# Optimization experiments

Hardware: AMD Instinct MI355X
Metric: run time of the kernel (lower is better)

## Reference

```python
import jax, jax.numpy as jnp
import numpy as np

N, E, F, H = 50000, 800000, 128, 128
HEADS, HOUT, NUM_GRAPHS, NUM_CLASSES, L = 4, 32, 50, 2, 3
BN_EPS = 1e-5


def setup_inputs() -> dict:
    key = jax.random.key(0)
    it = iter(jax.random.split(key, 64))
    def nrm(shape, scale=0.1):
        return scale * jax.random.normal(next(it), shape, jnp.float32)
    npg = N // NUM_GRAPHS  # nodes per graph = 1000
    # edges constrained to stay within a single graph
    src = jax.random.randint(next(it), (E,), 0, npg, jnp.int32)
    dst = jax.random.randint(next(it), (E,), 0, npg, jnp.int32)
    goff = jax.random.randint(next(it), (E,), 0, NUM_GRAPHS, jnp.int32) * npg
    return dict(
        x=jax.random.normal(next(it), (N, F), jnp.float32),
        edge_index=jnp.stack([src + goff, dst + goff]),
        batch=jnp.arange(N, dtype=jnp.int32) // npg,
        W_gcn=nrm((F, H)), b_gcn=nrm((H,)),
        gin_W1=nrm((F, H)), gin_b1=nrm((H,)), gin_W2=nrm((H, H)), gin_b2=nrm((H,)),
        W_gat=nrm((F, HEADS * HOUT)), b_gat=nrm((HEADS * HOUT,)),
        a_src=nrm((HEADS, HOUT)), a_dst=nrm((HEADS, HOUT)),
        gat_proj_W=nrm((HEADS * HOUT, H)), gat_proj_b=nrm((H,)),
        gate_W1=nrm((3 * H, H)), gate_b1=nrm((H,)), gate_W2=nrm((H, 3)), gate_b2=nrm((3,)),
        bn0_g=jnp.ones((H,), jnp.float32) + nrm((H,)), bn0_b=nrm((H,)),
        conv_rel_W=nrm((L, H, H)), conv_rel_b=nrm((L, H)), conv_root_W=nrm((L, H, H)),
        bn_g=jnp.ones((L, H), jnp.float32) + nrm((L, H)), bn_b=nrm((L, H)),
        jump_W=nrm((L * H, H)), jump_b=nrm((H,)),
        att_W1=nrm((H, H)), att_b1=nrm((H,)), att_W2=nrm((H, 1)), att_b2=nrm((1,)),
        comb_W=nrm((4 * H, H)), comb_b=nrm((H,)),
        cls_W1=nrm((H, H // 2)), cls_b1=nrm((H // 2,)),
        cls_W2=nrm((H // 2, NUM_CLASSES)), cls_b2=nrm((NUM_CLASSES,)),
    )


def _forward(x, edge_index, batch, W_gcn, b_gcn, gin_W1, gin_b1, gin_W2, gin_b2,
             W_gat, b_gat, a_src, a_dst, gat_proj_W, gat_proj_b,
             gate_W1, gate_b1, gate_W2, gate_b2, bn0_g, bn0_b,
             conv_rel_W, conv_rel_b, conv_root_W, bn_g, bn_b, jump_W, jump_b,
             att_W1, att_b1, att_W2, att_b2, comb_W, comb_b,
             cls_W1, cls_b1, cls_W2, cls_b2):
    relu = jax.nn.relu
    seg_sum, seg_max = jax.ops.segment_sum, jax.ops.segment_max
    n = x.shape[0]
    src, dst = edge_index[0], edge_index[1]
    loop = jnp.arange(n, dtype=src.dtype)
    src_sl = jnp.concatenate([src, loop])  # self-loops (GCN/GAT add them)
    dst_sl = jnp.concatenate([dst, loop])

    def bn(h, g, b):  # eval-mode BatchNorm1d, running mean=0, var=1
        return h * (g / jnp.sqrt(1.0 + BN_EPS)) + b

    # --- GCN stem: sym-normalized A+I ---
    deg = seg_sum(jnp.ones_like(dst_sl, jnp.float32), dst_sl, num_segments=n)
    dinv = jax.lax.rsqrt(deg)  # deg >= 1 thanks to self-loops
    norm = dinv[src_sl] * dinv[dst_sl]
    h = x @ W_gcn
    x_gcn = relu(seg_sum(h[src_sl] * norm[:, None], dst_sl, num_segments=n) + b_gcn)

    # --- GIN stem: MLP((1+0)*x + sum_j x_j), no self-loops ---
    aggr = seg_sum(x[src], dst, num_segments=n)
    x_gin = relu(relu((x + aggr) @ gin_W1 + gin_b1) @ gin_W2 + gin_b2)

    # --- GAT stem: per-edge attention, segment softmax over dst ---
    xp = (x @ W_gat).reshape(n, HEADS, HOUT)
    al_s = (xp * a_src).sum(-1)  # [n, heads]
    al_d = (xp * a_dst).sum(-1)
    e = jax.nn.leaky_relu(al_s[src_sl] + al_d[dst_sl], 0.2)  # [E+n, heads]
    m = seg_max(e, dst_sl, num_segments=n)
    ex = jnp.exp(e - m[dst_sl])
    alpha = ex / seg_sum(ex, dst_sl, num_segments=n)[dst_sl]
    x_gat = seg_sum(xp[src_sl] * alpha[:, :, None], dst_sl, num_segments=n)
    x_gat = x_gat.reshape(n, HEADS * HOUT) + b_gat
    x_gat = relu(x_gat) @ gat_proj_W + gat_proj_b

    # --- gated fusion ---
    x_cat = jnp.concatenate([x_gcn, x_gin, x_gat], axis=-1)
    gates = jax.nn.softmax(relu(x_cat @ gate_W1 + gate_b1) @ gate_W2 + gate_b2, axis=-1)
    xx = gates[:, 0:1] * x_gcn + gates[:, 1:2] * x_gin + gates[:, 2:3] * x_gat
    xx = relu(bn(xx, bn0_g, bn0_b))  # dropout = no-op in eval

    # --- GraphConv stack with residuals (IdentityPooling since use_sag=False) ---
    reps = []
    for i in range(L):
        x_in = xx
        a = seg_sum(xx[src], dst, num_segments=n)  # aggr='add'
        h = a @ conv_rel_W[i] + conv_rel_b[i] + xx @ conv_root_W[i]
        xx = relu(bn(h, bn_g[i], bn_b[i])) + x_in
        reps.append(xx)

    xx = jnp.concatenate(reps, axis=-1) @ jump_W + jump_b  # JK cat

    # --- combo global pooling: mean / max / add / att ---
    cnt = seg_sum(jnp.ones((n,), jnp.float32), batch, num_segments=NUM_GRAPHS)
    x_add = seg_sum(xx, batch, num_segments=NUM_GRAPHS)
    x_mean = x_add / cnt[:, None]
    x_max = seg_max(xx, batch, num_segments=NUM_GRAPHS)
    a_log = (relu(xx @ att_W1 + att_b1) @ att_W2 + att_b2)[:, 0]  # [n]
    mg = seg_max(a_log, batch, num_segments=NUM_GRAPHS)
    exg = jnp.exp(a_log - mg[batch])
    att = exg / seg_sum(exg, batch, num_segments=NUM_GRAPHS)[batch]
    x_att = seg_sum(xx * att[:, None], batch, num_segments=NUM_GRAPHS)
    hg = jnp.concatenate([x_mean, x_max, x_add, x_att], axis=-1) @ comb_W + comb_b

    return relu(hg @ cls_W1 + cls_b1) @ cls_W2 + cls_b2  # [NUM_GRAPHS, NUM_CLASSES]


def reference(x, edge_index, batch, W_gcn, b_gcn, gin_W1, gin_b1, gin_W2, gin_b2,
              W_gat, b_gat, a_src, a_dst, gat_proj_W, gat_proj_b,
              gate_W1, gate_b1, gate_W2, gate_b2, bn0_g, bn0_b,
              conv_rel_W, conv_rel_b, conv_root_W, bn_g, bn_b, jump_W, jump_b,
              att_W1, att_b1, att_W2, att_b2, comb_W, comb_b,
              cls_W1, cls_b1, cls_W2, cls_b2):
    return _forward(x, edge_index, batch, W_gcn, b_gcn, gin_W1, gin_b1, gin_W2, gin_b2,
                    W_gat, b_gat, a_src, a_dst, gat_proj_W, gat_proj_b,
                    gate_W1, gate_b1, gate_W2, gate_b2, bn0_g, bn0_b,
                    conv_rel_W, conv_rel_b, conv_root_W, bn_g, bn_b, jump_W, jump_b,
                    att_W1, att_b1, att_W2, att_b2, comb_W, comb_b,
                    cls_W1, cls_b1, cls_W2, cls_b2)
```

## Files before the change

kernel.cpp:

```cpp
#include <hip/hip_runtime.h>

typedef float f32x4 __attribute__((ext_vector_type(4)));
typedef short s16x8 __attribute__((ext_vector_type(8)));

#define LDA 136

static __device__ __forceinline__ unsigned short f2bf(float f){
  union { float f; unsigned int u; } v; v.f = f;
  unsigned int u = v.u;
  return (unsigned short)((u + 0x7fffu + ((u >> 16) & 1u)) >> 16);
}
static __device__ __forceinline__ float2 bfp2f(unsigned int p){
  union { unsigned int u; float f; } a, b;
  a.u = (p & 0xffffu) << 16; b.u = p & 0xffff0000u;
  return make_float2(a.f, b.f);
}
static __device__ __forceinline__ unsigned int f2bfp(float x, float y){
  return (unsigned int)f2bf(x) | ((unsigned int)f2bf(y) << 16);
}
static __device__ __forceinline__ float bf2f(unsigned short h){
  union { unsigned int u; float f; } v; v.u = (unsigned int)h << 16; return v.f;
}

static __device__ __forceinline__ float lrelu02(float x){ return x > 0.f ? x : 0.2f * x; }

static __device__ __forceinline__ int xcd_swz(int bid, int nwg){
  int q = nwg >> 3, r = nwg & 7, x = bid & 7, i = bid >> 3;
  return (x < r ? x * (q + 1) : r * (q + 1) + (x - r) * q) + i;
}


__global__ void zero_u32(unsigned int* p, int n){
  int i = blockIdx.x * 256 + threadIdx.x;
  if (i < n) p[i] = 0u;
}

__global__ void hist_kernel(const int* __restrict__ dst, unsigned int* __restrict__ cnt, int E){
  int i = blockIdx.x * 256 + threadIdx.x;
  if (i < E) atomicAdd(&cnt[dst[i]], 1u);
}

__global__ void scan1_kernel(const unsigned int* __restrict__ cnt, unsigned int* __restrict__ rp,
                             unsigned int* __restrict__ bsum, int n){
  __shared__ unsigned int s[1024];
  int b = blockIdx.x, tid = threadIdx.x, i = b * 1024 + tid;
  unsigned int v = (i < n) ? cnt[i] : 0u;
  s[tid] = v; __syncthreads();
  for (int off = 1; off < 1024; off <<= 1){
    unsigned int t = (tid >= off) ? s[tid - off] : 0u;
    __syncthreads();
    s[tid] += t;
    __syncthreads();
  }
  if (i < n) rp[i] = s[tid] - v;
  if (tid == 1023) bsum[b] = s[1023];
}

__global__ void scan2_kernel(unsigned int* __restrict__ bsum, int nb){
  __shared__ unsigned int s[256];
  int tid = threadIdx.x;
  unsigned int v = (tid < nb) ? bsum[tid] : 0u;
  s[tid] = v; __syncthreads();
  for (int off = 1; off < 256; off <<= 1){
    unsigned int t = (tid >= off) ? s[tid - off] : 0u;
    __syncthreads();
    s[tid] += t;
    __syncthreads();
  }
  if (tid < nb) bsum[tid] = s[tid] - v;
}

__global__ void scan3_kernel(unsigned int* __restrict__ rp, const unsigned int* __restrict__ bsum,
                             int n, unsigned int Etot){
  int i = blockIdx.x * 256 + threadIdx.x;
  if (i < n) rp[i] += bsum[i >> 10];
  if (i == 0) rp[n] = Etot;
}

__global__ void scatter_kernel(const int* __restrict__ src, const int* __restrict__ dst,
                               const unsigned int* __restrict__ rp, unsigned int* __restrict__ fill,
                               int* __restrict__ colA, int* __restrict__ cpos, int E){
  int i = blockIdx.x * 256 + threadIdx.x;
  if (i < E){
    int d = dst[i];
    unsigned int pos = rp[d] + atomicAdd(&fill[d], 1u);
    colA[pos] = src[i];
    cpos[i] = (int)pos;
  }
}

__global__ void dinv_kernel(const unsigned int* __restrict__ cnt, float* __restrict__ dinv, int n){
  int i = blockIdx.x * 256 + threadIdx.x;
  if (i < n) dinv[i] = rsqrtf((float)cnt[i] + 1.0f);
}

__global__ void xcast_kernel(const float* __restrict__ x, unsigned short* __restrict__ xb, int n2){
  int i = blockIdx.x * 256 + threadIdx.x;
  if (i < n2){
    float2 v = ((const float2*)x)[i];
    ((unsigned int*)xb)[i] = f2bfp(v.x, v.y);
  }
}

__global__ void ew_kernel(const int* __restrict__ src, const int* __restrict__ dst,
                          const int* __restrict__ cpos, const float* __restrict__ als,
                          const float* __restrict__ ald, float* __restrict__ wCSR, int E){
  int i = blockIdx.x * 256 + threadIdx.x;
  if (i >= E) return;
  int s = src[i], d = dst[i];
  float4 as = ((const float4*)als)[s];
  float4 ad = ((const float4*)ald)[d];
  float4 w;
  w.x = __expf(fminf(lrelu02(as.x + ad.x), 30.f));
  w.y = __expf(fminf(lrelu02(as.y + ad.y), 30.f));
  w.z = __expf(fminf(lrelu02(as.z + ad.z), 30.f));
  w.w = __expf(fminf(lrelu02(as.w + ad.w), 30.f));
  ((float4*)wCSR)[cpos[i]] = w;
}


struct WSrc { const float* p[18]; };

__global__ void wtrans_kernel(WSrc s, unsigned short* __restrict__ dstAll){
  const float* src = s.p[blockIdx.x];
  unsigned short* dst = dstAll + (size_t)blockIdx.x * 16384;
  __shared__ float st[64][129];
  int tid = threadIdx.x;
  int kb = blockIdx.y * 64;
#pragma unroll
  for (int j = 0; j < 8; ++j){
    int e = tid + 256 * j;
    int r = e >> 5, c4 = (e & 31) * 4;
    float4 v = *(const float4*)(src + (size_t)(kb + r) * 128 + c4);
    st[r][c4] = v.x; st[r][c4+1] = v.y; st[r][c4+2] = v.z; st[r][c4+3] = v.w;
  }
  __syncthreads();
#pragma unroll
  for (int j = 0; j < 8; ++j){
    int e = tid + 256 * j;
    int c = e >> 4, k4 = (e & 15) * 4;
    ushort4 o;
    o.x = f2bf(st[k4+0][c]); o.y = f2bf(st[k4+1][c]);
    o.z = f2bf(st[k4+2][c]); o.w = f2bf(st[k4+3][c]);
    *(ushort4*)(dst + (size_t)c * 128 + kb + k4) = o;
  }
}


template<int EPI>
__launch_bounds__(256, 2)
__global__ void gemm_kernel(const unsigned short* __restrict__ A0, const unsigned short* __restrict__ A1,
                            const unsigned short* __restrict__ A2,
                            const unsigned short* __restrict__ W0, const unsigned short* __restrict__ W1,
                            const unsigned short* __restrict__ W2,
                            const float* __restrict__ bias, const float* __restrict__ bng, const float* __restrict__ bnb,
                            const unsigned short* __restrict__ resid, unsigned short* __restrict__ C, int nrows)
{
  __shared__ unsigned short As[64 * LDA];
  __shared__ unsigned short Wt[128 * LDA];
  const int tid = threadIdx.x;
  const int wave = tid >> 6, lane = tid & 63;
  const int row0 = blockIdx.x * 64;
  const unsigned short* Aps[3] = {A0, A1, A2};
  const unsigned short* Wps[3] = {W0, W1, W2};
  f32x4 acc[8];
#pragma unroll
  for (int i = 0; i < 8; ++i) acc[i] = (f32x4){0.f, 0.f, 0.f, 0.f};

  for (int p = 0; p < 3; ++p){
    const unsigned short* Ap = Aps[p];
    if (Ap == nullptr) break;
    const unsigned short* Wp = Wps[p];
    if (p) __syncthreads();
#pragma unroll
    for (int j = 0; j < 4; ++j){
      int e = tid + 256 * j;
      int r = e >> 4, k8 = (e & 15) * 8;
      int gr = row0 + r;
      s16x8 v = {0,0,0,0,0,0,0,0};
      if (gr < nrows) v = *(const s16x8*)(Ap + (size_t)gr * 128 + k8);
      *(s16x8*)(As + r * LDA + k8) = v;
    }
#pragma unroll
    for (int j = 0; j < 8; ++j){
      int e = tid + 256 * j;
      int colw = e >> 4, k8 = (e & 15) * 8;
      *(s16x8*)(Wt + colw * LDA + k8) = *(const s16x8*)(Wp + (size_t)colw * 128 + k8);
    }
    __syncthreads();
#pragma unroll
    for (int kc = 0; kc < 4; ++kc){
      int ko = kc * 32 + (lane >> 4) * 8;
      s16x8 av = *(const s16x8*)(As + (wave * 16 + (lane & 15)) * LDA + ko);
#pragma unroll
      for (int ct = 0; ct < 8; ++ct){
        s16x8 bv = *(const s16x8*)(Wt + (ct * 16 + (lane & 15)) * LDA + ko);
        acc[ct] = __builtin_amdgcn_mfma_f32_16x16x32_bf16(av, bv, acc[ct], 0, 0, 0);
      }
    }
  }
  const float RSQ = 0.99999500003749969f;
#pragma unroll
  for (int ct = 0; ct < 8; ++ct){
    int colg = ct * 16 + (lane & 15);
    float bv_ = (EPI >= 1) ? bias[colg] : 0.f;
    float sg = (EPI == 3) ? bng[colg] * RSQ : 0.f;
    float sb = (EPI == 3) ? bnb[colg] : 0.f;
#pragma unroll
    for (int r = 0; r < 4; ++r){
      int rowg = row0 + wave * 16 + (lane >> 4) * 4 + r;
      if (rowg < nrows){
        float v = acc[ct][r];
        if (EPI == 1) v += bv_;
        else if (EPI == 2) v = fmaxf(v + bv_, 0.f);
        else if (EPI == 3){
          v = (v + bv_) * sg + sb;
          v = fmaxf(v, 0.f) + bf2f(resid[(size_t)rowg * 128 + colg]);
        }
        C[(size_t)rowg * 128 + colg] = f2bf(v);
      }
    }
  }
}

__launch_bounds__(256, 2)
__global__ void gemm_dual_kernel(const unsigned short* __restrict__ A,
                                 const unsigned short* __restrict__ W0, const unsigned short* __restrict__ W1,
                                 const float* __restrict__ dscale,
                                 unsigned short* __restrict__ C0, unsigned short* __restrict__ C1, int nrows)
{
  __shared__ unsigned short As[64 * LDA];
  __shared__ unsigned short Wt[128 * LDA];
  const int tid = threadIdx.x;
  const int wave = tid >> 6, lane = tid & 63;
  const int row0 = blockIdx.x * 64;
  f32x4 acc0[8], acc1[8];
#pragma unroll
  for (int i = 0; i < 8; ++i){ acc0[i] = (f32x4){0.f,0.f,0.f,0.f}; acc1[i] = (f32x4){0.f,0.f,0.f,0.f}; }

#pragma unroll
  for (int j = 0; j < 4; ++j){
    int e = tid + 256 * j;
    int r = e >> 4, k8 = (e & 15) * 8;
    int gr = row0 + r;
    s16x8 v = {0,0,0,0,0,0,0,0};
    if (gr < nrows) v = *(const s16x8*)(A + (size_t)gr * 128 + k8);
    *(s16x8*)(As + r * LDA + k8) = v;
  }
#pragma unroll
  for (int j = 0; j < 8; ++j){
    int e = tid + 256 * j;
    int colw = e >> 4, k8 = (e & 15) * 8;
    *(s16x8*)(Wt + colw * LDA + k8) = *(const s16x8*)(W0 + (size_t)colw * 128 + k8);
  }
  __syncthreads();
  s16x8 av[4];
#pragma unroll
  for (int kc = 0; kc < 4; ++kc)
    av[kc] = *(const s16x8*)(As + (wave * 16 + (lane & 15)) * LDA + kc * 32 + (lane >> 4) * 8);
#pragma unroll
  for (int kc = 0; kc < 4; ++kc){
    int ko = kc * 32 + (lane >> 4) * 8;
#pragma unroll
    for (int ct = 0; ct < 8; ++ct){
      s16x8 bv = *(const s16x8*)(Wt + (ct * 16 + (lane & 15)) * LDA + ko);
      acc0[ct] = __builtin_amdgcn_mfma_f32_16x16x32_bf16(av[kc], bv, acc0[ct], 0, 0, 0);
    }
  }
  __syncthreads();
#pragma unroll
  for (int j = 0; j < 8; ++j){
    int e = tid + 256 * j;
    int colw = e >> 4, k8 = (e & 15) * 8;
    *(s16x8*)(Wt + colw * LDA + k8) = *(const s16x8*)(W1 + (size_t)colw * 128 + k8);
  }
  __syncthreads();
#pragma unroll
  for (int kc = 0; kc < 4; ++kc){
    int ko = kc * 32 + (lane >> 4) * 8;
#pragma unroll
    for (int ct = 0; ct < 8; ++ct){
      s16x8 bv = *(const s16x8*)(Wt + (ct * 16 + (lane & 15)) * LDA + ko);
      acc1[ct] = __builtin_amdgcn_mfma_f32_16x16x32_bf16(av[kc], bv, acc1[ct], 0, 0, 0);
    }
  }
#pragma unroll
  for (int ct = 0; ct < 8; ++ct){
    int colg = ct * 16 + (lane & 15);
#pragma unroll
    for (int r = 0; r < 4; ++r){
      int rowg = row0 + wave * 16 + (lane >> 4) * 4 + r;
      if (rowg < nrows){
        C0[(size_t)rowg * 128 + colg] = f2bf(acc0[ct][r] * dscale[rowg]);
        C1[(size_t)rowg * 128 + colg] = f2bf(acc1[ct][r]);
      }
    }
  }
}


__global__ void gin_agg_kernel(const unsigned short* __restrict__ x, const unsigned int* __restrict__ rp,
                               const int* __restrict__ col, unsigned short* __restrict__ xs, int n){
  int bid = xcd_swz(blockIdx.x, gridDim.x);
  int node = bid * 4 + (int)(threadIdx.x >> 6);
  if (node >= n) return;
  int lane = threadIdx.x & 63;
  const unsigned int* xin = (const unsigned int*)x;
  float2 acc = bfp2f(xin[(size_t)node * 64 + lane]);
  unsigned int rs = rp[node], re = rp[node + 1], e = rs;
  for (; e + 4 <= re; e += 4){
    int s0 = col[e], s1 = col[e+1], s2 = col[e+2], s3 = col[e+3];
    float2 v0 = bfp2f(xin[(size_t)s0 * 64 + lane]);
    float2 v1 = bfp2f(xin[(size_t)s1 * 64 + lane]);
    float2 v2 = bfp2f(xin[(size_t)s2 * 64 + lane]);
    float2 v3 = bfp2f(xin[(size_t)s3 * 64 + lane]);
    acc.x += v0.x + v1.x + v2.x + v3.x;
    acc.y += v0.y + v1.y + v2.y + v3.y;
  }
  for (; e < re; ++e){
    float2 v = bfp2f(xin[(size_t)col[e] * 64 + lane]);
    acc.x += v.x; acc.y += v.y;
  }
  ((unsigned int*)xs)[(size_t)node * 64 + lane] = f2bfp(acc.x, acc.y);
}

__global__ void gcn_agg_kernel(const unsigned short* __restrict__ hd, const float* __restrict__ dinv,
                               const unsigned int* __restrict__ rp, const int* __restrict__ col,
                               const float* __restrict__ b, unsigned short* __restrict__ out, int n){
  int bid = xcd_swz(blockIdx.x, gridDim.x);
  int node = bid * 4 + (int)(threadIdx.x >> 6);
  if (node >= n) return;
  int lane = threadIdx.x & 63;
  const unsigned int* hv = (const unsigned int*)hd;
  float di = dinv[node];
  float2 acc = bfp2f(hv[(size_t)node * 64 + lane]);
  unsigned int rs = rp[node], re = rp[node + 1], e = rs;
  for (; e + 4 <= re; e += 4){
    int s0 = col[e], s1 = col[e+1], s2 = col[e+2], s3 = col[e+3];
    float2 v0 = bfp2f(hv[(size_t)s0 * 64 + lane]);
    float2 v1 = bfp2f(hv[(size_t)s1 * 64 + lane]);
    float2 v2 = bfp2f(hv[(size_t)s2 * 64 + lane]);
    float2 v3 = bfp2f(hv[(size_t)s3 * 64 + lane]);
    acc.x += v0.x + v1.x + v2.x + v3.x;
    acc.y += v0.y + v1.y + v2.y + v3.y;
  }
  for (; e < re; ++e){
    float2 v = bfp2f(hv[(size_t)col[e] * 64 + lane]);
    acc.x += v.x; acc.y += v.y;
  }
  int f = lane * 2;
  float o0 = fmaxf(acc.x * di + b[f], 0.f);
  float o1 = fmaxf(acc.y * di + b[f + 1], 0.f);
  ((unsigned int*)out)[(size_t)node * 64 + lane] = f2bfp(o0, o1);
}

__global__ void sum_agg_kernel(const unsigned short* __restrict__ x, const unsigned int* __restrict__ rp,
                               const int* __restrict__ col, unsigned short* __restrict__ out, int n){
  int bid = xcd_swz(blockIdx.x, gridDim.x);
  int node = bid * 4 + (int)(threadIdx.x >> 6);
  if (node >= n) return;
  int lane = threadIdx.x & 63;
  const unsigned int* xin = (const unsigned int*)x;
  float2 acc = make_float2(0.f, 0.f);
  unsigned int rs = rp[node], re = rp[node + 1], e = rs;
  for (; e + 4 <= re; e += 4){
    int s0 = col[e], s1 = col[e+1], s2 = col[e+2], s3 = col[e+3];
    float2 v0 = bfp2f(xin[(size_t)s0 * 64 + lane]);
    float2 v1 = bfp2f(xin[(size_t)s1 * 64 + lane]);
    float2 v2 = bfp2f(xin[(size_t)s2 * 64 + lane]);
    float2 v3 = bfp2f(xin[(size_t)s3 * 64 + lane]);
    acc.x += v0.x + v1.x + v2.x + v3.x;
    acc.y += v0.y + v1.y + v2.y + v3.y;
  }
  for (; e < re; ++e){
    float2 v = bfp2f(xin[(size_t)col[e] * 64 + lane]);
    acc.x += v.x; acc.y += v.y;
  }
  ((unsigned int*)out)[(size_t)node * 64 + lane] = f2bfp(acc.x, acc.y);
}

__global__ void gat_agg_kernel(const unsigned short* __restrict__ xp, const float* __restrict__ als,
                               const float* __restrict__ ald, const float* __restrict__ wCSR,
                               const unsigned int* __restrict__ rp, const int* __restrict__ col,
                               const float* __restrict__ bgat, unsigned short* __restrict__ out, int n){
  int bid = xcd_swz(blockIdx.x, gridDim.x);
  int node = bid * 4 + (int)(threadIdx.x >> 6);
  if (node >= n) return;
  int lane = threadIdx.x & 63;
  int h = lane >> 4;
  const unsigned int* xv = (const unsigned int*)xp;
  float w = __expf(fminf(lrelu02(als[(size_t)node * 4 + h] + ald[(size_t)node * 4 + h]), 30.f));
  float2 sv = bfp2f(xv[(size_t)node * 64 + lane]);
  float2 acc = make_float2(sv.x * w, sv.y * w);
  float denom = w;
  unsigned int rs = rp[node], re = rp[node + 1], e = rs;
  for (; e + 4 <= re; e += 4){
    int s0 = col[e], s1 = col[e+1], s2 = col[e+2], s3 = col[e+3];
    float w0 = wCSR[(size_t)(e+0) * 4 + h];
    float w1 = wCSR[(size_t)(e+1) * 4 + h];
    float w2 = wCSR[(size_t)(e+2) * 4 + h];
    float w3 = wCSR[(size_t)(e+3) * 4 + h];
    float2 v0 = bfp2f(xv[(size_t)s0 * 64 + lane]);
    float2 v1 = bfp2f(xv[(size_t)s1 * 64 + lane]);
    float2 v2 = bfp2f(xv[(size_t)s2 * 64 + lane]);
    float2 v3 = bfp2f(xv[(size_t)s3 * 64 + lane]);
    acc.x += v0.x * w0 + v1.x * w1 + v2.x * w2 + v3.x * w3;
    acc.y += v0.y * w0 + v1.y * w1 + v2.y * w2 + v3.y * w3;
    denom += w0 + w1 + w2 + w3;
  }
  for (; e < re; ++e){
    float we = wCSR[(size_t)e * 4 + h];
    float2 v = bfp2f(xv[(size_t)col[e] * 64 + lane]);
    acc.x += v.x * we; acc.y += v.y * we;
    denom += we;
  }
  float inv = 1.0f / denom;
  int f = lane * 2;
  float o0 = fmaxf(acc.x * inv + bgat[f], 0.f);
  float o1 = fmaxf(acc.y * inv + bgat[f + 1], 0.f);
  ((unsigned int*)out)[(size_t)node * 64 + lane] = f2bfp(o0, o1);
}


__global__ void alpair_kernel(const unsigned short* __restrict__ xp, const float* __restrict__ a_src,
                              const float* __restrict__ a_dst, float* __restrict__ als,
                              float* __restrict__ ald, int n){
  int node = blockIdx.x * 4 + (int)(threadIdx.x >> 6);
  if (node >= n) return;
  int lane = threadIdx.x & 63;
  int f = lane * 2;
  float2 v = bfp2f(((const unsigned int*)xp)[(size_t)node * 64 + lane]);
  float ps = v.x * a_src[f] + v.y * a_src[f + 1];
  float pd = v.x * a_dst[f] + v.y * a_dst[f + 1];
#pragma unroll
  for (int off = 1; off < 16; off <<= 1){
    ps += __shfl_xor(ps, off, 64);
    pd += __shfl_xor(pd, off, 64);
  }
  if ((lane & 15) == 0){
    int hh = lane >> 4;
    als[(size_t)node * 4 + hh] = ps;
    ald[(size_t)node * 4 + hh] = pd;
  }
}

__global__ void combine_kernel(const unsigned short* __restrict__ t, const float* __restrict__ W2,
                               const float* __restrict__ b2, const unsigned short* __restrict__ xg,
                               const unsigned short* __restrict__ xi, const unsigned short* __restrict__ xa,
                               const float* __restrict__ bn0g, const float* __restrict__ bn0b,
                               unsigned short* __restrict__ xx, int n){
  int node = blockIdx.x * 4 + (int)(threadIdx.x >> 6);
  if (node >= n) return;
  int lane = threadIdx.x & 63;
  int f = lane * 2;
  float2 tv = bfp2f(((const unsigned int*)t)[(size_t)node * 64 + lane]);
  float p0 = tv.x * W2[f * 3 + 0] + tv.y * W2[(f + 1) * 3 + 0];
  float p1 = tv.x * W2[f * 3 + 1] + tv.y * W2[(f + 1) * 3 + 1];
  float p2 = tv.x * W2[f * 3 + 2] + tv.y * W2[(f + 1) * 3 + 2];
#pragma unroll
  for (int off = 1; off < 64; off <<= 1){
    p0 += __shfl_xor(p0, off, 64);
    p1 += __shfl_xor(p1, off, 64);
    p2 += __shfl_xor(p2, off, 64);
  }
  p0 += b2[0]; p1 += b2[1]; p2 += b2[2];
  float mm = fmaxf(p0, fmaxf(p1, p2));
  float e0 = __expf(p0 - mm), e1 = __expf(p1 - mm), e2 = __expf(p2 - mm);
  float inv = 1.0f / (e0 + e1 + e2);
  e0 *= inv; e1 *= inv; e2 *= inv;
  float2 a = bfp2f(((const unsigned int*)xg)[(size_t)node * 64 + lane]);
  float2 b = bfp2f(((const unsigned int*)xi)[(size_t)node * 64 + lane]);
  float2 c = bfp2f(((const unsigned int*)xa)[(size_t)node * 64 + lane]);
  const float RSQ = 0.99999500003749969f;
  float o0 = fmaxf((e0 * a.x + e1 * b.x + e2 * c.x) * (bn0g[f] * RSQ) + bn0b[f], 0.f);
  float o1 = fmaxf((e0 * a.y + e1 * b.y + e2 * c.y) * (bn0g[f + 1] * RSQ) + bn0b[f + 1], 0.f);
  ((unsigned int*)xx)[(size_t)node * 64 + lane] = f2bfp(o0, o1);
}

__global__ void alog_kernel(const unsigned short* __restrict__ t, const float* __restrict__ w,
                            const float* __restrict__ b, float* __restrict__ alog, int n){
  int node = blockIdx.x * 4 + (int)(threadIdx.x >> 6);
  if (node >= n) return;
  int lane = threadIdx.x & 63;
  int f = lane * 2;
  float2 tv = bfp2f(((const unsigned int*)t)[(size_t)node * 64 + lane]);
  float p = tv.x * w[f] + tv.y * w[f + 1];
#pragma unroll
  for (int off = 1; off < 64; off <<= 1) p += __shfl_xor(p, off, 64);
  if (lane == 0) alog[node] = p + b[0];
}


__global__ void att_stats_kernel(const float* __restrict__ alog, float* __restrict__ gm,
                                 float* __restrict__ gz, int npg){
  __shared__ float red[256];
  int g = blockIdx.x, tid = threadIdx.x;
  size_t base = (size_t)g * npg;
  float m = -1e30f;
  for (int i = tid; i < npg; i += 256) m = fmaxf(m, alog[base + i]);
  red[tid] = m; __syncthreads();
  for (int off = 128; off > 0; off >>= 1){ if (tid < off) red[tid] = fmaxf(red[tid], red[tid + off]); __syncthreads(); }
  float gmax = red[0]; __syncthreads();
  float z = 0.f;
  for (int i = tid; i < npg; i += 256) z += __expf(alog[base + i] - gmax);
  red[tid] = z; __syncthreads();
  for (int off = 128; off > 0; off >>= 1){ if (tid < off) red[tid] += red[tid + off]; __syncthreads(); }
  if (tid == 0){ gm[g] = gmax; gz[g] = red[0]; }
}

__global__ void pool_partial_kernel(const unsigned short* __restrict__ xx, const float* __restrict__ alog,
                                    const float* __restrict__ gm, const float* __restrict__ gz,
                                    float* __restrict__ part, int npg, int nparts){
  __shared__ float wts[128];
  __shared__ float red[256];
  int g = blockIdx.x / nparts, p = blockIdx.x % nparts;
  int chunk = (npg + nparts - 1) / nparts;
  int n0 = p * chunk, n1 = min(npg, n0 + chunk);
  int tid = threadIdx.x;
  float gmax = gm[g], ginv = 1.0f / gz[g];
  size_t base = (size_t)g * npg;
  for (int i = n0 + tid; i < n1; i += 256) wts[i - n0] = __expf(alog[base + i] - gmax) * ginv;
  __syncthreads();
  int f = tid & 127, half = tid >> 7;
  float add = 0.f, mx = -1e30f, att = 0.f;
  for (int n2 = n0 + half; n2 < n1; n2 += 2){
    float v = bf2f(xx[(base + n2) * 128 + f]);
    add += v; mx = fmaxf(mx, v); att += v * wts[n2 - n0];
  }
  red[tid] = add; __syncthreads();
  float addf = add + ((half == 0) ? red[tid + 128] : 0.f);
  __syncthreads(); red[tid] = mx; __syncthreads();
  float mxf = (half == 0) ? fmaxf(mx, red[tid + 128]) : 0.f;
  __syncthreads(); red[tid] = att; __syncthreads();
  float attf = att + ((half == 0) ? red[tid + 128] : 0.f);
  if (half == 0){
    float* o = part + (size_t)(g * nparts + p) * 384;
    o[f] = addf; o[128 + f] = mxf; o[256 + f] = attf;
  }
}

__global__ void pool_final_kernel(const float* __restrict__ part, float* __restrict__ hg,
                                  int npg, int nparts){
  int g = blockIdx.x, f = threadIdx.x;
  float add = 0.f, mx = -1e30f, att = 0.f;
  for (int p = 0; p < nparts; ++p){
    const float* o = part + (size_t)(g * nparts + p) * 384;
    add += o[f]; mx = fmaxf(mx, o[128 + f]); att += o[256 + f];
  }
  float* o = hg + (size_t)g * 512;
  o[f] = add / (float)npg;
  o[128 + f] = mx;
  o[256 + f] = add;
  o[384 + f] = att;
}

__global__ void head_kernel(const float* __restrict__ hg, const float* __restrict__ combW,
                            const float* __restrict__ combB, const float* __restrict__ c1W,
                            const float* __restrict__ c1B, const float* __restrict__ c2W,
                            const float* __restrict__ c2B, float* __restrict__ out){
  __shared__ float cat[512];
  __shared__ float h1[128];
  __shared__ float h2[64];
  int g = blockIdx.x, tid = threadIdx.x;
#pragma unroll
  for (int j = 0; j < 4; ++j) cat[tid + 128 * j] = hg[(size_t)g * 512 + tid + 128 * j];
  __syncthreads();
  float a = combB[tid];
  for (int k = 0; k < 512; ++k) a += cat[k] * combW[(size_t)k * 128 + tid];
  h1[tid] = a; __syncthreads();
  if (tid < 64){
    float b = c1B[tid];
    for (int k = 0; k < 128; ++k) b += h1[k] * c1W[(size_t)k * 64 + tid];
    h2[tid] = fmaxf(b, 0.f);
  }
  __syncthreads();
  if (tid < 2){
    float o = c2B[tid];
    for (int k = 0; k < 64; ++k) o += h2[k] * c2W[(size_t)k * 2 + tid];
    out[(size_t)g * 2 + tid] = o;
  }
}


static void launch_gemm(int epi, dim3 grid, hipStream_t st,
                        const unsigned short* A0, const unsigned short* A1, const unsigned short* A2,
                        const unsigned short* W0, const unsigned short* W1, const unsigned short* W2,
                        const float* bias, const float* bng, const float* bnb,
                        const unsigned short* resid, unsigned short* C, int nrows){
  switch (epi){
    case 0: gemm_kernel<0><<<grid, 256, 0, st>>>(A0, A1, A2, W0, W1, W2, bias, bng, bnb, resid, C, nrows); break;
    case 1: gemm_kernel<1><<<grid, 256, 0, st>>>(A0, A1, A2, W0, W1, W2, bias, bng, bnb, resid, C, nrows); break;
    case 2: gemm_kernel<2><<<grid, 256, 0, st>>>(A0, A1, A2, W0, W1, W2, bias, bng, bnb, resid, C, nrows); break;
    default: gemm_kernel<3><<<grid, 256, 0, st>>>(A0, A1, A2, W0, W1, W2, bias, bng, bnb, resid, C, nrows); break;
  }
}

extern "C" void kernel_launch(void* const* d_in, const int* in_sizes, int n_in,
                              void* d_out, int out_size, void* d_ws, size_t ws_size,
                              hipStream_t stream){
  (void)n_in; (void)out_size; (void)ws_size;
  const int N = in_sizes[0] / 128;
  const int E = in_sizes[1] / 2;
  const int NG = 50;
  const int npg = N / NG;

  const float* x       = (const float*)d_in[0];
  const int*   ei      = (const int*)d_in[1];
  const int*   srcI    = ei;
  const int*   dstI    = ei + E;
  const float* W_gcn   = (const float*)d_in[3];
  const float* b_gcn   = (const float*)d_in[4];
  const float* gin_W1  = (const float*)d_in[5];
  const float* gin_b1  = (const float*)d_in[6];
  const float* gin_W2  = (const float*)d_in[7];
  const float* gin_b2  = (const float*)d_in[8];
  const float* W_gat   = (const float*)d_in[9];
  const float* b_gat   = (const float*)d_in[10];
  const float* a_src   = (const float*)d_in[11];
  const float* a_dst   = (const float*)d_in[12];
  const float* gproj_W = (const float*)d_in[13];
  const float* gproj_b = (const float*)d_in[14];
  const float* gate_W1 = (const float*)d_in[15];
  const float* gate_b1 = (const float*)d_in[16];
  const float* gate_W2 = (const float*)d_in[17];
  const float* gate_b2 = (const float*)d_in[18];
  const float* bn0_g   = (const float*)d_in[19];
  const float* bn0_b   = (const float*)d_in[20];
  const float* rel_W   = (const float*)d_in[21];
  const float* rel_b   = (const float*)d_in[22];
  const float* root_W  = (const float*)d_in[23];
  const float* bn_g    = (const float*)d_in[24];
  const float* bn_b    = (const float*)d_in[25];
  const float* jump_W  = (const float*)d_in[26];
  const float* jump_b  = (const float*)d_in[27];
  const float* att_W1  = (const float*)d_in[28];
  const float* att_b1  = (const float*)d_in[29];
  const float* att_W2  = (const float*)d_in[30];
  const float* att_b2  = (const float*)d_in[31];
  const float* comb_W  = (const float*)d_in[32];
  const float* comb_b  = (const float*)d_in[33];
  const float* cls_W1  = (const float*)d_in[34];
  const float* cls_b1  = (const float*)d_in[35];
  const float* cls_W2  = (const float*)d_in[36];
  const float* cls_b2  = (const float*)d_in[37];
  float* out = (float*)d_out;

  char* wp = (char*)d_ws;
  auto alloc = [&](size_t b) -> char* {
    char* p = wp; wp += (b + 511) & ~(size_t)511; return p;
  };
  unsigned int* cnt  = (unsigned int*)alloc((size_t)N * 4);
  unsigned int* fill = (unsigned int*)alloc((size_t)N * 4);
  unsigned int* rp   = (unsigned int*)alloc(((size_t)N + 1) * 4);
  int* colA          = (int*)alloc((size_t)E * 4);
  int* cpos          = (int*)alloc((size_t)E * 4);
  float* wCSR        = (float*)alloc((size_t)E * 16);
  unsigned int* bsum = (unsigned int*)alloc(256 * 4);
  float* dinv        = (float*)alloc((size_t)N * 4);
  float* als         = (float*)alloc((size_t)N * 16);
  float* ald         = (float*)alloc((size_t)N * 16);
  float* alogv       = (float*)alloc((size_t)N * 4);
  unsigned short* WtAll = (unsigned short*)alloc((size_t)18 * 16384 * 2);
  float* hg          = (float*)alloc((size_t)NG * 512 * 4);
  float* gmv         = (float*)alloc((size_t)NG * 4);
  float* gzv         = (float*)alloc((size_t)NG * 4);
  int nparts = (npg + 99) / 100;
  float* part        = (float*)alloc((size_t)NG * nparts * 384 * 4);
  unsigned short* xbf = (unsigned short*)alloc((size_t)N * 128 * 2);
  unsigned short* S0 = (unsigned short*)alloc((size_t)N * 128 * 2);
  unsigned short* S1 = (unsigned short*)alloc((size_t)N * 128 * 2);
  unsigned short* S2 = (unsigned short*)alloc((size_t)N * 128 * 2);
  unsigned short* S3 = (unsigned short*)alloc((size_t)N * 128 * 2);
  unsigned short* S4 = (unsigned short*)alloc((size_t)N * 128 * 2);

  int zn = (int)(((char*)rp - (char*)cnt) / 4);
  zero_u32<<<(zn + 255) / 256, 256, 0, stream>>>(cnt, zn);
  hist_kernel<<<(E + 255) / 256, 256, 0, stream>>>(dstI, cnt, E);
  int nbScan = (N + 1023) / 1024;
  scan1_kernel<<<nbScan, 1024, 0, stream>>>(cnt, rp, bsum, N);
  scan2_kernel<<<1, 256, 0, stream>>>(bsum, nbScan);
  scan3_kernel<<<(N + 255) / 256, 256, 0, stream>>>(rp, bsum, N, (unsigned int)E);
  scatter_kernel<<<(E + 255) / 256, 256, 0, stream>>>(srcI, dstI, rp, fill, colA, cpos, E);
  dinv_kernel<<<(N + 255) / 256, 256, 0, stream>>>(cnt, dinv, N);

  WSrc wsrc;
  wsrc.p[0] = W_gcn;  wsrc.p[1] = W_gat;  wsrc.p[2] = gin_W1; wsrc.p[3] = gin_W2;
  wsrc.p[4] = gproj_W;
  wsrc.p[5] = gate_W1;      wsrc.p[6] = gate_W1 + 16384; wsrc.p[7] = gate_W1 + 32768;
  wsrc.p[8] = rel_W;        wsrc.p[9] = rel_W + 16384;   wsrc.p[10] = rel_W + 32768;
  wsrc.p[11] = root_W;      wsrc.p[12] = root_W + 16384; wsrc.p[13] = root_W + 32768;
  wsrc.p[14] = jump_W;      wsrc.p[15] = jump_W + 16384; wsrc.p[16] = jump_W + 32768;
  wsrc.p[17] = att_W1;
  wtrans_kernel<<<dim3(18, 2), 256, 0, stream>>>(wsrc, WtAll);
  xcast_kernel<<<(N * 64 + 255) / 256, 256, 0, stream>>>(x, xbf, N * 64);

  dim3 gg((N + 63) / 64);
  int nb4 = (N + 3) / 4;
  #define WT(i) (WtAll + (size_t)(i) * 16384)
  const unsigned short* Z = nullptr;
  const unsigned short* BZ = nullptr;

  gemm_dual_kernel<<<gg, 256, 0, stream>>>(xbf, WT(0), WT(1), dinv, S0, S1, N);
  alpair_kernel<<<nb4, 256, 0, stream>>>(S1, a_src, a_dst, als, ald, N);
  ew_kernel<<<(E + 255) / 256, 256, 0, stream>>>(srcI, dstI, cpos, als, ald, wCSR, E);
  gin_agg_kernel<<<nb4, 256, 0, stream>>>(xbf, rp, colA, S2, N);
  launch_gemm(2, gg, stream, S2, BZ, BZ, WT(2), Z, Z, gin_b1, nullptr, nullptr, BZ, S3, N);
  launch_gemm(2, gg, stream, S3, BZ, BZ, WT(3), Z, Z, gin_b2, nullptr, nullptr, BZ, S2, N);
  gcn_agg_kernel<<<nb4, 256, 0, stream>>>(S0, dinv, rp, colA, b_gcn, S3, N);
  gat_agg_kernel<<<nb4, 256, 0, stream>>>(S1, als, ald, wCSR, rp, colA, b_gat, S0, N);
  launch_gemm(1, gg, stream, S0, BZ, BZ, WT(4), Z, Z, gproj_b, nullptr, nullptr, BZ, S1, N);

  launch_gemm(2, gg, stream, S3, S2, S1, WT(5), WT(6), WT(7), gate_b1, nullptr, nullptr, BZ, S4, N);
  combine_kernel<<<nb4, 256, 0, stream>>>(S4, gate_W2, gate_b2, S3, S2, S1, bn0_g, bn0_b, S0, N);

  sum_agg_kernel<<<nb4, 256, 0, stream>>>(S0, rp, colA, S1, N);
  launch_gemm(3, gg, stream, S1, S0, BZ, WT(8), WT(11), Z, rel_b, bn_g, bn_b, S0, S2, N);
  sum_agg_kernel<<<nb4, 256, 0, stream>>>(S2, rp, colA, S1, N);
  launch_gemm(3, gg, stream, S1, S2, BZ, WT(9), WT(12), Z, rel_b + 128, bn_g + 128, bn_b + 128, S2, S3, N);
  sum_agg_kernel<<<nb4, 256, 0, stream>>>(S3, rp, colA, S1, N);
  launch_gemm(3, gg, stream, S1, S3, BZ, WT(10), WT(13), Z, rel_b + 256, bn_g + 256, bn_b + 256, S3, S4, N);

  launch_gemm(1, gg, stream, S2, S3, S4, WT(14), WT(15), WT(16), jump_b, nullptr, nullptr, BZ, S0, N);
  launch_gemm(2, gg, stream, S0, BZ, BZ, WT(17), Z, Z, att_b1, nullptr, nullptr, BZ, S1, N);
  alog_kernel<<<nb4, 256, 0, stream>>>(S1, att_W2, att_b2, alogv, N);

  att_stats_kernel<<<NG, 256, 0, stream>>>(alogv, gmv, gzv, npg);
  pool_partial_kernel<<<NG * nparts, 256, 0, stream>>>(S0, alogv, gmv, gzv, part, npg, nparts);
  pool_final_kernel<<<NG, 128, 0, stream>>>(part, hg, npg, nparts);
  head_kernel<<<NG, 128, 0, stream>>>(hg, comb_W, comb_b, cls_W1, cls_b1, cls_W2, cls_b2, out);
}
```

Baseline: 693.1 us.

## Build CSR per graph with two-level bucketing and store GAT edge weights in bf16

Replaces the global histogram, three-pass scan and atomic scatter with per-graph bucketing. Edges are first bucketed by graph, then each graph's CSR is built in one block using shared-memory histograms and a block scan, which also writes dinv and a per-edge destination array. The edge-weight kernel now walks edges in CSR order (no cpos indirection) and stores the four head weights as bf16. This cuts global atomics, kernel launches and edge-weight bandwidth. In exchange it relies on edges never crossing graphs and on npg being at most 1024, and it loses precision in the attention weights.

```diff
diff --git a/kernel.cpp b/kernel.cpp
--- a/kernel.cpp
+++ b/kernel.cpp
@@ -35,63 +35,88 @@
   if (i < n) p[i] = 0u;
 }
 
-__global__ void hist_kernel(const int* __restrict__ dst, unsigned int* __restrict__ cnt, int E){
-  int i = blockIdx.x * 256 + threadIdx.x;
-  if (i < E) atomicAdd(&cnt[dst[i]], 1u);
-}
-
-__global__ void scan1_kernel(const unsigned int* __restrict__ cnt, unsigned int* __restrict__ rp,
-                             unsigned int* __restrict__ bsum, int n){
-  __shared__ unsigned int s[1024];
-  int b = blockIdx.x, tid = threadIdx.x, i = b * 1024 + tid;
-  unsigned int v = (i < n) ? cnt[i] : 0u;
-  s[tid] = v; __syncthreads();
+__global__ void gcount_kernel(const int* __restrict__ dst, unsigned int* __restrict__ gcnt,
+                              int E, int npg, int ng){
+  __shared__ unsigned int h[64];
+  int tid = threadIdx.x;
+  if (tid < 64) h[tid] = 0u;
+  __syncthreads();
+  for (int i = blockIdx.x * 256 + tid; i < E; i += gridDim.x * 256)
+    atomicAdd(&h[dst[i] / npg], 1u);
+  __syncthreads();
+  if (tid < ng) atomicAdd(&gcnt[tid], h[tid]);
+}
+
+__global__ void gscan_kernel(const unsigned int* __restrict__ gcnt, unsigned int* __restrict__ goff, int ng){
+  if (threadIdx.x == 0){
+    unsigned int run = 0;
+    for (int i = 0; i < ng; ++i){ goff[i] = run; run += gcnt[i]; }
+    goff[ng] = run;
+  }
+}
+
+__global__ void gbucket_kernel(const int* __restrict__ src, const int* __restrict__ dst,
+                               const unsigned int* __restrict__ goff, unsigned int* __restrict__ gfill,
+                               int2* __restrict__ ebuf, int E, int npg, int ng){
+  __shared__ unsigned int h[64];
+  __shared__ unsigned int base[64];
+  __shared__ unsigned int fl[64];
+  int tid = threadIdx.x;
+  if (tid < 64){ h[tid] = 0u; fl[tid] = 0u; }
+  __syncthreads();
+  int per = (E + gridDim.x - 1) / gridDim.x;
+  int i0 = blockIdx.x * per, i1 = min(E, i0 + per);
+  for (int i = i0 + tid; i < i1; i += 256)
+    atomicAdd(&h[dst[i] / npg], 1u);
+  __syncthreads();
+  if (tid < ng) base[tid] = goff[tid] + atomicAdd(&gfill[tid], h[tid]);
+  __syncthreads();
+  for (int i = i0 + tid; i < i1; i += 256){
+    int d = dst[i];
+    int g = d / npg;
+    unsigned int p = base[g] + atomicAdd(&fl[g], 1u);
+    ebuf[p] = make_int2(src[i], d);
+  }
+}
+
+__global__ void csr_graph_kernel(const int2* __restrict__ ebuf, const unsigned int* __restrict__ goff,
+                                 unsigned int* __restrict__ rp, int* __restrict__ colA,
+                                 int* __restrict__ dstA, float* __restrict__ dinv,
+                                 int npg, int N, int Etot){
+  __shared__ unsigned int hist[1024];
+  __shared__ unsigned int fill[1024];
+  int g = blockIdx.x, tid = threadIdx.x;
+  unsigned int e0 = goff[g], e1 = goff[g + 1];
+  int nbase = g * npg;
+  hist[tid] = 0u; fill[tid] = 0u;
+  __syncthreads();
+  for (unsigned int e = e0 + tid; e < e1; e += 1024)
+    atomicAdd(&hist[ebuf[e].y - nbase], 1u);
+  __syncthreads();
+  unsigned int cnt = hist[tid];
   for (int off = 1; off < 1024; off <<= 1){
-    unsigned int t = (tid >= off) ? s[tid - off] : 0u;
+    unsigned int t = (tid >= off) ? hist[tid - off] : 0u;
     __syncthreads();
-    s[tid] += t;
+    hist[tid] += t;
     __syncthreads();
   }
-  if (i < n) rp[i] = s[tid] - v;
-  if (tid == 1023) bsum[b] = s[1023];
-}
-
-__global__ void scan2_kernel(unsigned int* __restrict__ bsum, int nb){
-  __shared__ unsigned int s[256];
-  int tid = threadIdx.x;
-  unsigned int v = (tid < nb) ? bsum[tid] : 0u;
-  s[tid] = v; __syncthreads();
-  for (int off = 1; off < 256; off <<= 1){
-    unsigned int t = (tid >= off) ? s[tid - off] : 0u;
-    __syncthreads();
-    s[tid] += t;
-    __syncthreads();
-  }
-  if (tid < nb) bsum[tid] = s[tid] - v;
-}
-
-__global__ void scan3_kernel(unsigned int* __restrict__ rp, const unsigned int* __restrict__ bsum,
-                             int n, unsigned int Etot){
-  int i = blockIdx.x * 256 + threadIdx.x;
-  if (i < n) rp[i] += bsum[i >> 10];
-  if (i == 0) rp[n] = Etot;
-}
-
-__global__ void scatter_kernel(const int* __restrict__ src, const int* __restrict__ dst,
-                               const unsigned int* __restrict__ rp, unsigned int* __restrict__ fill,
-                               int* __restrict__ colA, int* __restrict__ cpos, int E){
-  int i = blockIdx.x * 256 + threadIdx.x;
-  if (i < E){
-    int d = dst[i];
-    unsigned int pos = rp[d] + atomicAdd(&fill[d], 1u);
-    colA[pos] = src[i];
-    cpos[i] = (int)pos;
-  }
-}
-
-__global__ void dinv_kernel(const unsigned int* __restrict__ cnt, float* __restrict__ dinv, int n){
-  int i = blockIdx.x * 256 + threadIdx.x;
-  if (i < n) dinv[i] = rsqrtf((float)cnt[i] + 1.0f);
+  unsigned int basev = e0 + hist[tid] - cnt;
+  __syncthreads();
+  hist[tid] = basev;
+  if (tid < npg){
+    int node = nbase + tid;
+    rp[node] = basev;
+    dinv[node] = rsqrtf((float)cnt + 1.0f);
+  }
+  if (g == 0 && tid == 0) rp[N] = (unsigned int)Etot;
+  __syncthreads();
+  for (unsigned int e = e0 + tid; e < e1; e += 1024){
+    int2 sd = ebuf[e];
+    int ld = sd.y - nbase;
+    unsigned int pos = hist[ld] + atomicAdd(&fill[ld], 1u);
+    colA[pos] = sd.x;
+    dstA[pos] = sd.y;
+  }
 }
 
 __global__ void xcast_kernel(const float* __restrict__ x, unsigned short* __restrict__ xb, int n2){
@@ -102,20 +127,20 @@
   }
 }
 
-__global__ void ew_kernel(const int* __restrict__ src, const int* __restrict__ dst,
-                          const int* __restrict__ cpos, const float* __restrict__ als,
-                          const float* __restrict__ ald, float* __restrict__ wCSR, int E){
+__global__ void ew_kernel(const int* __restrict__ colA, const int* __restrict__ dstA,
+                          const float* __restrict__ als, const float* __restrict__ ald,
+                          unsigned int* __restrict__ wb, int E){
   int i = blockIdx.x * 256 + threadIdx.x;
   if (i >= E) return;
-  int s = src[i], d = dst[i];
+  int s = colA[i], d = dstA[i];
   float4 as = ((const float4*)als)[s];
   float4 ad = ((const float4*)ald)[d];
-  float4 w;
-  w.x = __expf(fminf(lrelu02(as.x + ad.x), 30.f));
-  w.y = __expf(fminf(lrelu02(as.y + ad.y), 30.f));
-  w.z = __expf(fminf(lrelu02(as.z + ad.z), 30.f));
-  w.w = __expf(fminf(lrelu02(as.w + ad.w), 30.f));
-  ((float4*)wCSR)[cpos[i]] = w;
+  float w0 = __expf(fminf(lrelu02(as.x + ad.x), 30.f));
+  float w1 = __expf(fminf(lrelu02(as.y + ad.y), 30.f));
+  float w2 = __expf(fminf(lrelu02(as.z + ad.z), 30.f));
+  float w3 = __expf(fminf(lrelu02(as.w + ad.w), 30.f));
+  wb[(size_t)i * 2 + 0] = f2bfp(w0, w1);
+  wb[(size_t)i * 2 + 1] = f2bfp(w2, w3);
 }
 
 
@@ -380,7 +405,7 @@
 }
 
 __global__ void gat_agg_kernel(const unsigned short* __restrict__ xp, const float* __restrict__ als,
-                               const float* __restrict__ ald, const float* __restrict__ wCSR,
+                               const float* __restrict__ ald, const unsigned int* __restrict__ wb,
                                const unsigned int* __restrict__ rp, const int* __restrict__ col,
                                const float* __restrict__ bgat, unsigned short* __restrict__ out, int n){
   int bid = xcd_swz(blockIdx.x, gridDim.x);
@@ -388,6 +413,7 @@
   if (node >= n) return;
   int lane = threadIdx.x & 63;
   int h = lane >> 4;
+  int wword = h >> 1, wsh = (h & 1) * 16;
   const unsigned int* xv = (const unsigned int*)xp;
   float w = __expf(fminf(lrelu02(als[(size_t)node * 4 + h] + ald[(size_t)node * 4 + h]), 30.f));
   float2 sv = bfp2f(xv[(size_t)node * 64 + lane]);
@@ -396,10 +422,10 @@
   unsigned int rs = rp[node], re = rp[node + 1], e = rs;
   for (; e + 4 <= re; e += 4){
     int s0 = col[e], s1 = col[e+1], s2 = col[e+2], s3 = col[e+3];
-    float w0 = wCSR[(size_t)(e+0) * 4 + h];
-    float w1 = wCSR[(size_t)(e+1) * 4 + h];
-    float w2 = wCSR[(size_t)(e+2) * 4 + h];
-    float w3 = wCSR[(size_t)(e+3) * 4 + h];
+    float w0 = bf2f((unsigned short)(wb[(size_t)(e+0) * 2 + wword] >> wsh));
+    float w1 = bf2f((unsigned short)(wb[(size_t)(e+1) * 2 + wword] >> wsh));
+    float w2 = bf2f((unsigned short)(wb[(size_t)(e+2) * 2 + wword] >> wsh));
+    float w3 = bf2f((unsigned short)(wb[(size_t)(e+3) * 2 + wword] >> wsh));
     float2 v0 = bfp2f(xv[(size_t)s0 * 64 + lane]);
     float2 v1 = bfp2f(xv[(size_t)s1 * 64 + lane]);
     float2 v2 = bfp2f(xv[(size_t)s2 * 64 + lane]);
@@ -409,7 +435,7 @@
     denom += w0 + w1 + w2 + w3;
   }
   for (; e < re; ++e){
-    float we = wCSR[(size_t)e * 4 + h];
+    float we = bf2f((unsigned short)(wb[(size_t)e * 2 + wword] >> wsh));
     float2 v = bfp2f(xv[(size_t)col[e] * 64 + lane]);
     acc.x += v.x * we; acc.y += v.y * we;
     denom += we;
@@ -649,13 +675,14 @@
   auto alloc = [&](size_t b) -> char* {
     char* p = wp; wp += (b + 511) & ~(size_t)511; return p;
   };
-  unsigned int* cnt  = (unsigned int*)alloc((size_t)N * 4);
-  unsigned int* fill = (unsigned int*)alloc((size_t)N * 4);
   unsigned int* rp   = (unsigned int*)alloc(((size_t)N + 1) * 4);
   int* colA          = (int*)alloc((size_t)E * 4);
-  int* cpos          = (int*)alloc((size_t)E * 4);
-  float* wCSR        = (float*)alloc((size_t)E * 16);
-  unsigned int* bsum = (unsigned int*)alloc(256 * 4);
+  int* dstA          = (int*)alloc((size_t)E * 4);
+  int2* ebuf         = (int2*)alloc((size_t)E * 8);
+  unsigned int* wb   = (unsigned int*)alloc((size_t)E * 8);
+  unsigned int* gcnt = (unsigned int*)alloc(192 * 4);
+  unsigned int* gfill= gcnt + 64;
+  unsigned int* goff = gcnt + 128;
   float* dinv        = (float*)alloc((size_t)N * 4);
   float* als         = (float*)alloc((size_t)N * 16);
   float* ald         = (float*)alloc((size_t)N * 16);
@@ -673,15 +700,11 @@
   unsigned short* S3 = (unsigned short*)alloc((size_t)N * 128 * 2);
   unsigned short* S4 = (unsigned short*)alloc((size_t)N * 128 * 2);
 
-  int zn = (int)(((char*)rp - (char*)cnt) / 4);
-  zero_u32<<<(zn + 255) / 256, 256, 0, stream>>>(cnt, zn);
-  hist_kernel<<<(E + 255) / 256, 256, 0, stream>>>(dstI, cnt, E);
-  int nbScan = (N + 1023) / 1024;
-  scan1_kernel<<<nbScan, 1024, 0, stream>>>(cnt, rp, bsum, N);
-  scan2_kernel<<<1, 256, 0, stream>>>(bsum, nbScan);
-  scan3_kernel<<<(N + 255) / 256, 256, 0, stream>>>(rp, bsum, N, (unsigned int)E);
-  scatter_kernel<<<(E + 255) / 256, 256, 0, stream>>>(srcI, dstI, rp, fill, colA, cpos, E);
-  dinv_kernel<<<(N + 255) / 256, 256, 0, stream>>>(cnt, dinv, N);
+  zero_u32<<<1, 256, 0, stream>>>(gcnt, 128);
+  gcount_kernel<<<256, 256, 0, stream>>>(dstI, gcnt, E, npg, NG);
+  gscan_kernel<<<1, 64, 0, stream>>>(gcnt, goff, NG);
+  gbucket_kernel<<<256, 256, 0, stream>>>(srcI, dstI, goff, gfill, ebuf, E, npg, NG);
+  csr_graph_kernel<<<NG, 1024, 0, stream>>>(ebuf, goff, rp, colA, dstA, dinv, npg, N, E);
 
   WSrc wsrc;
   wsrc.p[0] = W_gcn;  wsrc.p[1] = W_gat;  wsrc.p[2] = gin_W1; wsrc.p[3] = gin_W2;
@@ -702,12 +725,12 @@
 
   gemm_dual_kernel<<<gg, 256, 0, stream>>>(xbf, WT(0), WT(1), dinv, S0, S1, N);
   alpair_kernel<<<nb4, 256, 0, stream>>>(S1, a_src, a_dst, als, ald, N);
-  ew_kernel<<<(E + 255) / 256, 256, 0, stream>>>(srcI, dstI, cpos, als, ald, wCSR, E);
+  ew_kernel<<<(E + 255) / 256, 256, 0, stream>>>(colA, dstA, als, ald, wb, E);
   gin_agg_kernel<<<nb4, 256, 0, stream>>>(xbf, rp, colA, S2, N);
   launch_gemm(2, gg, stream, S2, BZ, BZ, WT(2), Z, Z, gin_b1, nullptr, nullptr, BZ, S3, N);
   launch_gemm(2, gg, stream, S3, BZ, BZ, WT(3), Z, Z, gin_b2, nullptr, nullptr, BZ, S2, N);
   gcn_agg_kernel<<<nb4, 256, 0, stream>>>(S0, dinv, rp, colA, b_gcn, S3, N);
-  gat_agg_kernel<<<nb4, 256, 0, stream>>>(S1, als, ald, wCSR, rp, colA, b_gat, S0, N);
+  gat_agg_kernel<<<nb4, 256, 0, stream>>>(S1, als, ald, wb, rp, colA, b_gat, S0, N);
   launch_gemm(1, gg, stream, S0, BZ, BZ, WT(4), Z, Z, gproj_b, nullptr, nullptr, BZ, S1, N);
 
   launch_gemm(2, gg, stream, S3, S2, S1, WT(5), WT(6), WT(7), gate_b1, nullptr, nullptr, BZ, S4, N);
```

After: 653.9 us. 1.06x faster.
